# Kernel optimization log

Hardware: AMD Instinct MI355X
Metric: run time of the kernel (lower is better)

## Reference

```python
import jax, jax.numpy as jnp
from jax import lax
import numpy as np

HIDDEN = 512
INPUT = 64
ALPHA = 1.0 / 10.0  # dt / tau = 1.0 / 10.0


def setup_inputs() -> dict:
    key = jax.random.key(0)
    k1, k2, k3, k4, k5, k6 = jax.random.split(key, 6)
    inputs = jax.random.normal(k1, (64, INPUT), dtype=jnp.float32)
    # Linear params (torch convention: y = x @ W.T + b)
    W_in = jax.random.normal(k2, (HIDDEN, INPUT), dtype=jnp.float32) / np.sqrt(INPUT)
    b_in = jax.random.normal(k3, (HIDDEN,), dtype=jnp.float32) * 0.01
    W_rec = jax.random.normal(k4, (HIDDEN, HIDDEN), dtype=jnp.float32) / np.sqrt(HIDDEN)
    w_out = jax.random.normal(k5, (1, HIDDEN), dtype=jnp.float32) / np.sqrt(HIDDEN)
    b_out = jax.random.normal(k6, (1,), dtype=jnp.float32) * 0.01
    return {
        "inputs": inputs,
        "W_in": W_in,
        "b_in": b_in,
        "W_rec": W_rec,
        "w_out": w_out,
        "b_out": b_out,
        "warmup_steps": 100,
        "response_steps": 400,
        "num_trials": 8,
    }


def reference(inputs, W_in, b_in, W_rec, w_out, b_out, warmup_steps, response_steps, num_trials):
    batch_size = inputs.shape[0]
    # expand each batch row num_trials times (matches unsqueeze/expand/reshape)
    x = jnp.repeat(inputs, num_trials, axis=0)  # [B*T_trials, I]
    input_contribution = x @ W_in.T + b_in      # [E, H]
    h0 = jnp.zeros((batch_size * num_trials, HIDDEN), dtype=inputs.dtype)

    def step(h, _):
        rec = jax.nn.softplus(h) @ W_rec.T
        h = h * (1.0 - ALPHA) + ALPHA * (rec + input_contribution)
        return h, None

    h, _ = lax.scan(step, h0, None, length=warmup_steps)

    def step_collect(h, _):
        rec = jax.nn.softplus(h) @ W_rec.T
        h = h * (1.0 - ALPHA) + ALPHA * (rec + input_contribution)
        return h, h

    _, hs = lax.scan(step_collect, h, None, length=response_steps)  # [S, E, H]

    out = hs @ w_out[0] + b_out[0]            # [S, E]
    hazard = jax.nn.sigmoid(out)
    # [S, E] -> [E, S] -> [batch, trials, steps]
    hazard = hazard.T.reshape(batch_size, num_trials, response_steps)
    return hazard
```

## Files before the change

### kernel.cpp

```cpp
#include <hip/hip_runtime.h>
#include <math.h>

#define HIDDEN 512
#define INPUT  64
#define NB     64
#define NT     8
#define WARM   100
#define RESP   400
#define ALPHA  0.1f

#define NREGC  23
#define NLDSC  9

typedef _Float16 half8  __attribute__((ext_vector_type(8)));
typedef _Float16 half2v __attribute__((ext_vector_type(2)));

#if defined(__has_builtin)
#  if __has_builtin(__builtin_amdgcn_fdot2)
#    define HAS_FDOT2 1
#  endif
#endif

__device__ __forceinline__ void dot8(half8 w, half8 s, float& a0, float& a1) {
#ifdef HAS_FDOT2
  a0 = __builtin_amdgcn_fdot2(__builtin_shufflevector(w, w, 0, 1),
                              __builtin_shufflevector(s, s, 0, 1), a0, false);
  a1 = __builtin_amdgcn_fdot2(__builtin_shufflevector(w, w, 2, 3),
                              __builtin_shufflevector(s, s, 2, 3), a1, false);
  a0 = __builtin_amdgcn_fdot2(__builtin_shufflevector(w, w, 4, 5),
                              __builtin_shufflevector(s, s, 4, 5), a0, false);
  a1 = __builtin_amdgcn_fdot2(__builtin_shufflevector(w, w, 6, 7),
                              __builtin_shufflevector(s, s, 6, 7), a1, false);
#else
#pragma unroll
  for (int l = 0; l < 8; ++l)
    ((l & 1) ? a1 : a0) = fmaf((float)w[l], (float)s[l], (l & 1) ? a1 : a0);
#endif
}

__device__ __forceinline__ void dot8f(float w0, float w1, float w2, float w3,
                                      half8 s, float& a0, float& a1) {
#ifdef HAS_FDOT2
  a0 = __builtin_amdgcn_fdot2(__builtin_bit_cast(half2v, w0),
                              __builtin_shufflevector(s, s, 0, 1), a0, false);
  a1 = __builtin_amdgcn_fdot2(__builtin_bit_cast(half2v, w1),
                              __builtin_shufflevector(s, s, 2, 3), a1, false);
  a0 = __builtin_amdgcn_fdot2(__builtin_bit_cast(half2v, w2),
                              __builtin_shufflevector(s, s, 4, 5), a0, false);
  a1 = __builtin_amdgcn_fdot2(__builtin_bit_cast(half2v, w3),
                              __builtin_shufflevector(s, s, 6, 7), a1, false);
#else
  const float wf[4] = {w0, w1, w2, w3};
#pragma unroll
  for (int p = 0; p < 4; ++p) {
    half2v wp = __builtin_bit_cast(half2v, wf[p]);
    float& a = (p & 1) ? a1 : a0;
    a = fmaf((float)wp[0], (float)s[2 * p], a);
    a = fmaf((float)wp[1], (float)s[2 * p + 1], a);
  }
#endif
}

__global__ void convert_w_pack_kernel(const float* __restrict__ W,
                                      _Float16* __restrict__ Wpk) {
  const int t = blockIdx.x * blockDim.x + threadIdx.x;
  const int kblk = t & 63;
  const int j = t >> 6;
  const float* src = W + (size_t)j * HIDDEN + kblk * 8;
  _Float16* dst = Wpk + ((size_t)kblk * HIDDEN + j) * 8;
#pragma unroll
  for (int l = 0; l < 8; ++l) dst[l] = (_Float16)src[l];
}

__global__ void
__attribute__((amdgpu_flat_work_group_size(1024, 1024), amdgpu_waves_per_eu(4, 4)))
leaky_rnn_res_kernel(const float* __restrict__ inputs,
                     const float* __restrict__ W_in,
                     const float* __restrict__ b_in,
                     const _Float16* __restrict__ Wpk,
                     const float* __restrict__ w_out,
                     const float* __restrict__ b_out,
                     float* __restrict__ out ) {
  const int b = blockIdx.x;
  const int t = threadIdx.x;
  const int j = t & (HIDDEN - 1);
  const int kh = t >> 9;

  __shared__ __align__(16) half8 ldsW[NLDSC][1024];
  __shared__ __align__(16) _Float16 sp_h[HIDDEN];
  __shared__ float xin[INPUT];
  __shared__ float redk[HIDDEN];
  __shared__ float wsum[8];

  const half8* __restrict__ Wp8 =
      (const half8*)Wpk + (size_t)(kh * 32) * HIDDEN + j;
  const float4* __restrict__ Wp4 = (const float4*)Wp8;

  float wrf[NREGC * 4];
#pragma unroll
  for (int c = 0; c < NREGC; ++c) {
    float4 v = Wp4[(size_t)c * HIDDEN];
    wrf[4 * c + 0] = v.x;
    wrf[4 * c + 1] = v.y;
    wrf[4 * c + 2] = v.z;
    wrf[4 * c + 3] = v.w;
    asm volatile("" : "+v"(wrf[4 * c + 0]), "+v"(wrf[4 * c + 1]),
                      "+v"(wrf[4 * c + 2]), "+v"(wrf[4 * c + 3]));
  }
#pragma unroll
  for (int c = 0; c < NLDSC; ++c) ldsW[c][t] = Wp8[(size_t)(NREGC + c) * HIDDEN];

  if (t < INPUT) xin[t] = inputs[b * INPUT + t];
  __syncthreads();

  float ic = 0.f, wout = 0.f;
  const float bout = b_out[0];
  if (t < HIDDEN) {
    ic = b_in[j];
    const float* wi = W_in + (size_t)j * INPUT;
#pragma unroll
    for (int i = 0; i < INPUT; ++i) ic = fmaf(xin[i], wi[i], ic);
    wout = w_out[j];
    sp_h[j] = (_Float16)0.6931471805599453f;
  }
  float h = 0.f;
  __syncthreads();

  const half8* sp8 = ((const half8*)sp_h) + kh * 32;
  float* const ob = out + (size_t)b * (NT * RESP) + (t < NT ? t * RESP : 0);

  for (int step = 0; step < WARM + RESP; ++step) {
    float acc0 = 0.f, acc1 = 0.f;
#pragma unroll
    for (int c = 0; c < NLDSC; ++c) {
      half8 w = ldsW[c][t];
      half8 s = sp8[NREGC + c];
      dot8(w, s, acc0, acc1);
    }
#pragma unroll
    for (int c = 0; c < NREGC; ++c) {
      half8 s = sp8[c];
      dot8f(wrf[4 * c + 0], wrf[4 * c + 1], wrf[4 * c + 2], wrf[4 * c + 3],
            s, acc0, acc1);
    }
    const float acc = acc0 + acc1;

    if (t >= HIDDEN) redk[j] = acc;
    __syncthreads();

    if (t < HIDDEN) {
      const float rec = acc + redk[j];
      h = h * (1.f - ALPHA) + ALPHA * (rec + ic);
      const float sp = fmaxf(h, 0.f) + log1pf(expf(-fabsf(h)));
      sp_h[j] = (_Float16)sp;
      if (step >= WARM) {
        float v = h * wout;
#pragma unroll
        for (int off = 32; off > 0; off >>= 1) v += __shfl_down(v, off);
        if ((t & 63) == 0) wsum[t >> 6] = v;
      }
    }
    __syncthreads();

    if (step >= WARM && t < NT) {
      float o = bout;
#pragma unroll
      for (int w = 0; w < 8; ++w) o += wsum[w];
      const float hz = 1.f / (1.f + expf(-o));
      ob[step - WARM] = hz;
    }
  }
}

__global__ void __launch_bounds__(512, 1)
leaky_rnn_row_kernel(const float* __restrict__ inputs,
                     const float* __restrict__ W_in,
                     const float* __restrict__ b_in,
                     const float* __restrict__ W_rec,
                     const float* __restrict__ w_out,
                     const float* __restrict__ b_out,
                     float* __restrict__ out) {
  const int b = blockIdx.x;
  const int j = threadIdx.x;
  __shared__ float sp[HIDDEN];
  __shared__ float xin[INPUT];
  __shared__ float red[8];
  if (j < INPUT) xin[j] = inputs[b * INPUT + j];
  __syncthreads();
  float ic = b_in[j];
  const float* wi = W_in + j * INPUT;
#pragma unroll
  for (int i = 0; i < INPUT; ++i) ic = fmaf(xin[i], wi[i], ic);
  const float wout = w_out[j];
  const float bout = b_out[0];
  float h = 0.0f;
  sp[j] = 0.6931471805599453f;
  __syncthreads();
  const float4* __restrict__ Wr = (const float4*)(W_rec + (size_t)j * HIDDEN);
  for (int step = 0; step < WARM + RESP; ++step) {
    float rec = 0.0f;
#pragma unroll 8
    for (int k4 = 0; k4 < HIDDEN / 4; ++k4) {
      float4 w = Wr[k4];
      float4 s = *(const float4*)&sp[4 * k4];
      rec = fmaf(w.x, s.x, rec);
      rec = fmaf(w.y, s.y, rec);
      rec = fmaf(w.z, s.z, rec);
      rec = fmaf(w.w, s.w, rec);
    }
    h = h * (1.0f - ALPHA) + ALPHA * (rec + ic);
    if (step >= WARM) {
      float v = h * wout;
#pragma unroll
      for (int off = 32; off > 0; off >>= 1) v += __shfl_down(v, off);
      if ((j & 63) == 0) red[j >> 6] = v;
    }
    __syncthreads();
    sp[j] = fmaxf(h, 0.0f) + log1pf(expf(-fabsf(h)));
    if (step >= WARM && j == 0) {
      float o = bout;
#pragma unroll
      for (int w = 0; w < 8; ++w) o += red[w];
      const float hz = 1.0f / (1.0f + expf(-o));
      const int s = step - WARM;
      float* obp = out + (size_t)b * (NT * RESP) + s;
#pragma unroll
      for (int tr = 0; tr < NT; ++tr) obp[tr * RESP] = hz;
    }
    __syncthreads();
  }
}

extern "C" void kernel_launch(void* const* d_in, const int* in_sizes, int n_in,
                              void* d_out, int out_size, void* d_ws, size_t ws_size,
                              hipStream_t stream) {
  const float* inputs = (const float*)d_in[0];
  const float* W_in   = (const float*)d_in[1];
  const float* b_in   = (const float*)d_in[2];
  const float* W_rec  = (const float*)d_in[3];
  const float* w_out  = (const float*)d_in[4];
  const float* b_out  = (const float*)d_in[5];
  float* out = (float*)d_out;

  const int nW = HIDDEN * HIDDEN;
  if (ws_size >= (size_t)nW * sizeof(_Float16)) {
    _Float16* Wpk = (_Float16*)d_ws;
    convert_w_pack_kernel<<<dim3(HIDDEN * 64 / 256), dim3(256), 0, stream>>>(W_rec, Wpk);
    leaky_rnn_res_kernel<<<dim3(NB), dim3(2 * HIDDEN), 0, stream>>>(
        inputs, W_in, b_in, Wpk, w_out, b_out, out);
  } else {
    leaky_rnn_row_kernel<<<dim3(NB), dim3(HIDDEN), 0, stream>>>(
        inputs, W_in, b_in, W_rec, w_out, b_out, out);
  }
}
```

Measured before the change: 1.085 ms.

## Split each batch row across four workgroups with global-memory flag synchronization

Adds a quad kernel where each batch row is handled by four cooperating workgroups, each owning 128 hidden units with its fp16 slice of W_rec fully resident in LDS. Every step the workgroups exchange softplus values and partial output sums through global memory, using relaxed atomics and per-step flag spinning. This spreads the work over 256 workgroups instead of 64 and removes the register-held weight tile. The cost is a cross-workgroup round trip through global memory every step, and it relies on all 256 workgroups being resident at once to avoid deadlock; the spin loop has a guard that breaks out after a bounded count.

```diff
diff --git a/kernel.cpp b/kernel.cpp
--- a/kernel.cpp
+++ b/kernel.cpp
@@ -7,10 +7,8 @@
 #define NT     8
 #define WARM   100
 #define RESP   400
+#define STEPS  (WARM + RESP)
 #define ALPHA  0.1f
-
-#define NREGC  23
-#define NLDSC  9
 
 typedef _Float16 half8  __attribute__((ext_vector_type(8)));
 typedef _Float16 half2v __attribute__((ext_vector_type(2)));
@@ -36,6 +34,148 @@
   for (int l = 0; l < 8; ++l)
     ((l & 1) ? a1 : a0) = fmaf((float)w[l], (float)s[l], (l & 1) ? a1 : a0);
 #endif
+}
+
+#define OFF_W    0
+#define OFF_SPEX (512 * 1024)
+#define OFF_OSUM (OFF_SPEX + NB * HIDDEN * 4)
+#define OFF_FLAG (OFF_OSUM + 1024)
+#define WS_NEED  (OFF_FLAG + 1024)
+
+__global__ void stage_quad_kernel(const float* __restrict__ W,
+                                  _Float16* __restrict__ Wst) {
+  const int gid = blockIdx.x * blockDim.x + threadIdx.x;
+  const int q  = gid >> 13;
+  const int c  = (gid >> 10) & 7;
+  const int tm = gid & 1023;
+  const int jg = q * 128 + (tm >> 3);
+  const int kb = (tm & 7) * 64 + c * 8;
+  const float* src = W + (size_t)jg * HIDDEN + kb;
+  _Float16* dst = Wst + ((size_t)(q * 8 + c) * 1024 + tm) * 8;
+#pragma unroll
+  for (int l = 0; l < 8; ++l) dst[l] = (_Float16)src[l];
+}
+
+__global__ void __launch_bounds__(1024)
+leaky_rnn_quad_kernel(const float* __restrict__ inputs,
+                      const float* __restrict__ W_in,
+                      const float* __restrict__ b_in,
+                      const _Float16* __restrict__ Wst,
+                      const float* __restrict__ w_out,
+                      const float* __restrict__ b_out,
+                      unsigned* __restrict__ sp_ex,
+                      unsigned* __restrict__ osum_ex,
+                      unsigned* __restrict__ flags,
+                      float* __restrict__ out ) {
+  const int wg = blockIdx.x;
+  const int r = wg & 63;
+  const int q = wg >> 6;
+  const int t = threadIdx.x;
+  const int jl = t >> 3;
+  const int kq = t & 7;
+  const int jg = q * 128 + jl;
+
+  __shared__ __align__(16) _Float16 ldsW[8 * 1024 * 8];
+  __shared__ __align__(16) _Float16 spst[2][8 * 72];
+  __shared__ float xin[INPUT];
+  __shared__ float wsum[16];
+
+  half8* ldsW8 = (half8*)ldsW;
+  const half8* Ws = (const half8*)Wst + (size_t)q * 8 * 1024;
+#pragma unroll
+  for (int c = 0; c < 8; ++c) ldsW8[c * 1024 + t] = Ws[c * 1024 + t];
+
+  if (t < INPUT) xin[t] = inputs[r * INPUT + t];
+  if (t < 8 * 72) spst[0][t] = (_Float16)0.6931471805599453f;
+  __syncthreads();
+
+  float ic = b_in[jg];
+  const float* wi = W_in + (size_t)jg * INPUT;
+#pragma unroll
+  for (int i = 0; i < INPUT; ++i) ic = fmaf(xin[i], wi[i], ic);
+  const float wout = w_out[jg];
+  const float bout = b_out[0];
+  float h = 0.f;
+
+  unsigned* const spex_r = sp_ex + r * HIDDEN;
+  unsigned* const osum_r = osum_ex + r * 4;
+  unsigned* const flag_r = flags + r * 4;
+  float* const ob = out + (size_t)r * (NT * RESP);
+
+  for (int step = 0; step < STEPS; ++step) {
+    const int p = step & 1;
+    const _Float16* spg = &spst[p][kq * 72];
+
+    float a0 = 0.f, a1 = 0.f;
+#pragma unroll
+    for (int c = 0; c < 8; ++c) {
+      half8 w = ldsW8[c * 1024 + t];
+      half8 s = *(const half8*)(spg + c * 8);
+      dot8(w, s, a0, a1);
+    }
+    float d = a0 + a1;
+    d += __shfl_xor(d, 1);
+    d += __shfl_xor(d, 2);
+    d += __shfl_xor(d, 4);
+
+    h = h * (1.f - ALPHA) + ALPHA * (d + ic);
+    const float spf = fmaxf(h, 0.f) + log1pf(expf(-fabsf(h)));
+
+    if (kq == 0) {
+      spst[1 - p][(jg >> 6) * 72 + (jg & 63)] = (_Float16)spf;
+      __hip_atomic_store(&spex_r[jg], __builtin_bit_cast(unsigned, spf),
+                         __ATOMIC_RELAXED, __HIP_MEMORY_SCOPE_AGENT);
+    }
+    if (step >= WARM) {
+      float v = (kq == 0) ? h * wout : 0.f;
+#pragma unroll
+      for (int off = 32; off; off >>= 1) v += __shfl_down(v, off);
+      if ((t & 63) == 0) wsum[t >> 6] = v;
+    }
+    __syncthreads();
+
+    if (t == 0) {
+      if (step >= WARM) {
+        float os = 0.f;
+#pragma unroll
+        for (int w = 0; w < 16; ++w) os += wsum[w];
+        __hip_atomic_store(&osum_r[q], __builtin_bit_cast(unsigned, os),
+                           __ATOMIC_RELAXED, __HIP_MEMORY_SCOPE_AGENT);
+      }
+      asm volatile("s_waitcnt vmcnt(0)" ::: "memory");
+      __hip_atomic_store(&flag_r[q], (unsigned)(step + 1),
+                         __ATOMIC_RELAXED, __HIP_MEMORY_SCOPE_AGENT);
+    }
+    if (t < 3) {
+      const int pq = t + (t >= q ? 1 : 0);
+      long guard = 0;
+      while (__hip_atomic_load(&flag_r[pq], __ATOMIC_RELAXED,
+                               __HIP_MEMORY_SCOPE_AGENT) <= (unsigned)step) {
+        if (++guard > (1L << 27)) break;
+      }
+    }
+    __syncthreads();
+
+    if (t < 384) {
+      const int k = t + (t >= q * 128 ? 128 : 0);
+      unsigned u = __hip_atomic_load(&spex_r[k], __ATOMIC_RELAXED,
+                                     __HIP_MEMORY_SCOPE_AGENT);
+      spst[1 - p][(k >> 6) * 72 + (k & 63)] =
+          (_Float16)__builtin_bit_cast(float, u);
+    }
+    if (step >= WARM && q == 0 && t == 0) {
+      float o = bout;
+#pragma unroll
+      for (int qq = 0; qq < 4; ++qq)
+        o += __builtin_bit_cast(
+            float, __hip_atomic_load(&osum_r[qq], __ATOMIC_RELAXED,
+                                     __HIP_MEMORY_SCOPE_AGENT));
+      const float hz = 1.f / (1.f + expf(-o));
+#pragma unroll
+      for (int tr = 0; tr < NT; ++tr) ob[tr * RESP + (step - WARM)] = hz;
+    }
+    __syncthreads();
+  }
 }
 
 __device__ __forceinline__ void dot8f(float w0, float w1, float w2, float w3,
@@ -52,14 +192,17 @@
 #else
   const float wf[4] = {w0, w1, w2, w3};
 #pragma unroll
-  for (int p = 0; p < 4; ++p) {
-    half2v wp = __builtin_bit_cast(half2v, wf[p]);
-    float& a = (p & 1) ? a1 : a0;
-    a = fmaf((float)wp[0], (float)s[2 * p], a);
-    a = fmaf((float)wp[1], (float)s[2 * p + 1], a);
+  for (int pp = 0; pp < 4; ++pp) {
+    half2v wp = __builtin_bit_cast(half2v, wf[pp]);
+    float& a = (pp & 1) ? a1 : a0;
+    a = fmaf((float)wp[0], (float)s[2 * pp], a);
+    a = fmaf((float)wp[1], (float)s[2 * pp + 1], a);
   }
 #endif
 }
+
+#define NREGC 23
+#define NLDSC 9
 
 __global__ void convert_w_pack_kernel(const float* __restrict__ W,
                                       _Float16* __restrict__ Wpk) {
@@ -72,15 +215,14 @@
   for (int l = 0; l < 8; ++l) dst[l] = (_Float16)src[l];
 }
 
-__global__ void
-__attribute__((amdgpu_flat_work_group_size(1024, 1024), amdgpu_waves_per_eu(4, 4)))
+__global__ void __launch_bounds__(1024)
 leaky_rnn_res_kernel(const float* __restrict__ inputs,
                      const float* __restrict__ W_in,
                      const float* __restrict__ b_in,
                      const _Float16* __restrict__ Wpk,
                      const float* __restrict__ w_out,
                      const float* __restrict__ b_out,
-                     float* __restrict__ out ) {
+                     float* __restrict__ out) {
   const int b = blockIdx.x;
   const int t = threadIdx.x;
   const int j = t & (HIDDEN - 1);
@@ -100,10 +242,8 @@
 #pragma unroll
   for (int c = 0; c < NREGC; ++c) {
     float4 v = Wp4[(size_t)c * HIDDEN];
-    wrf[4 * c + 0] = v.x;
-    wrf[4 * c + 1] = v.y;
-    wrf[4 * c + 2] = v.z;
-    wrf[4 * c + 3] = v.w;
+    wrf[4 * c + 0] = v.x; wrf[4 * c + 1] = v.y;
+    wrf[4 * c + 2] = v.z; wrf[4 * c + 3] = v.w;
     asm volatile("" : "+v"(wrf[4 * c + 0]), "+v"(wrf[4 * c + 1]),
                       "+v"(wrf[4 * c + 2]), "+v"(wrf[4 * c + 3]));
   }
@@ -129,21 +269,15 @@
   const half8* sp8 = ((const half8*)sp_h) + kh * 32;
   float* const ob = out + (size_t)b * (NT * RESP) + (t < NT ? t * RESP : 0);
 
-  for (int step = 0; step < WARM + RESP; ++step) {
-    float acc0 = 0.f, acc1 = 0.f;
-#pragma unroll
-    for (int c = 0; c < NLDSC; ++c) {
-      half8 w = ldsW[c][t];
-      half8 s = sp8[NREGC + c];
-      dot8(w, s, acc0, acc1);
-    }
-#pragma unroll
-    for (int c = 0; c < NREGC; ++c) {
-      half8 s = sp8[c];
+  for (int step = 0; step < STEPS; ++step) {
+    float a0 = 0.f, a1 = 0.f;
+#pragma unroll
+    for (int c = 0; c < NLDSC; ++c) dot8(ldsW[c][t], sp8[NREGC + c], a0, a1);
+#pragma unroll
+    for (int c = 0; c < NREGC; ++c)
       dot8f(wrf[4 * c + 0], wrf[4 * c + 1], wrf[4 * c + 2], wrf[4 * c + 3],
-            s, acc0, acc1);
-    }
-    const float acc = acc0 + acc1;
+            sp8[c], a0, a1);
+    const float acc = a0 + a1;
 
     if (t >= HIDDEN) redk[j] = acc;
     __syncthreads();
@@ -151,8 +285,7 @@
     if (t < HIDDEN) {
       const float rec = acc + redk[j];
       h = h * (1.f - ALPHA) + ALPHA * (rec + ic);
-      const float sp = fmaxf(h, 0.f) + log1pf(expf(-fabsf(h)));
-      sp_h[j] = (_Float16)sp;
+      sp_h[j] = (_Float16)(fmaxf(h, 0.f) + log1pf(expf(-fabsf(h))));
       if (step >= WARM) {
         float v = h * wout;
 #pragma unroll
@@ -166,8 +299,7 @@
       float o = bout;
 #pragma unroll
       for (int w = 0; w < 8; ++w) o += wsum[w];
-      const float hz = 1.f / (1.f + expf(-o));
-      ob[step - WARM] = hz;
+      ob[step - WARM] = 1.f / (1.f + expf(-o));
     }
   }
 }
@@ -197,16 +329,14 @@
   sp[j] = 0.6931471805599453f;
   __syncthreads();
   const float4* __restrict__ Wr = (const float4*)(W_rec + (size_t)j * HIDDEN);
-  for (int step = 0; step < WARM + RESP; ++step) {
+  for (int step = 0; step < STEPS; ++step) {
     float rec = 0.0f;
 #pragma unroll 8
     for (int k4 = 0; k4 < HIDDEN / 4; ++k4) {
       float4 w = Wr[k4];
       float4 s = *(const float4*)&sp[4 * k4];
-      rec = fmaf(w.x, s.x, rec);
-      rec = fmaf(w.y, s.y, rec);
-      rec = fmaf(w.z, s.z, rec);
-      rec = fmaf(w.w, s.w, rec);
+      rec = fmaf(w.x, s.x, rec); rec = fmaf(w.y, s.y, rec);
+      rec = fmaf(w.z, s.z, rec); rec = fmaf(w.w, s.w, rec);
     }
     h = h * (1.0f - ALPHA) + ALPHA * (rec + ic);
     if (step >= WARM) {
@@ -222,8 +352,7 @@
 #pragma unroll
       for (int w = 0; w < 8; ++w) o += red[w];
       const float hz = 1.0f / (1.0f + expf(-o));
-      const int s = step - WARM;
-      float* obp = out + (size_t)b * (NT * RESP) + s;
+      float* obp = out + (size_t)b * (NT * RESP) + (step - WARM);
 #pragma unroll
       for (int tr = 0; tr < NT; ++tr) obp[tr * RESP] = hz;
     }
@@ -242,8 +371,17 @@
   const float* b_out  = (const float*)d_in[5];
   float* out = (float*)d_out;
 
-  const int nW = HIDDEN * HIDDEN;
-  if (ws_size >= (size_t)nW * sizeof(_Float16)) {
+  if (ws_size >= (size_t)WS_NEED) {
+    char* ws = (char*)d_ws;
+    _Float16* Wst  = (_Float16*)(ws + OFF_W);
+    unsigned* spex = (unsigned*)(ws + OFF_SPEX);
+    unsigned* osum = (unsigned*)(ws + OFF_OSUM);
+    unsigned* flg  = (unsigned*)(ws + OFF_FLAG);
+    hipMemsetAsync(flg, 0, NB * 4 * sizeof(unsigned), stream);
+    stage_quad_kernel<<<dim3(128), dim3(256), 0, stream>>>(W_rec, Wst);
+    leaky_rnn_quad_kernel<<<dim3(256), dim3(1024), 0, stream>>>(
+        inputs, W_in, b_in, Wst, w_out, b_out, spex, osum, flg, out);
+  } else if (ws_size >= (size_t)HIDDEN * HIDDEN * sizeof(_Float16)) {
     _Float16* Wpk = (_Float16*)d_ws;
     convert_w_pack_kernel<<<dim3(HIDDEN * 64 / 256), dim3(256), 0, stream>>>(W_rec, Wpk);
     leaky_rnn_res_kernel<<<dim3(NB), dim3(2 * HIDDEN), 0, stream>>>(
```

After: 1.762 ms. +62.5%, slower.

## Split recurrent weights across AGPRs, global streaming, and LDS

Applied to the files above, without the earlier changes.

Weight residency changes. Before, 23 half8 chunks per thread sat in VGPRs and 9 in LDS. Now 16 chunks sit in AGPRs, read back with v_accvgpr_read each step, and 7 chunks are re-streamed from global/L2 every timestep, while LDS still holds 9. The aim is to free VGPR pressure and the waves_per_eu constraint. The cost is extra accvgpr reads, and per-step global loads that sit on the serial recurrence critical path.

```diff
diff --git a/kernel.cpp b/kernel.cpp
--- a/kernel.cpp
+++ b/kernel.cpp
@@ -7,9 +7,11 @@
 #define NT     8
 #define WARM   100
 #define RESP   400
+#define STEPS  (WARM + RESP)
 #define ALPHA  0.1f
 
-#define NREGC  23
+#define NAGPC  16
+#define NSTRC  7
 #define NLDSC  9
 
 typedef _Float16 half8  __attribute__((ext_vector_type(8)));
@@ -61,6 +63,15 @@
 #endif
 }
 
+__device__ __forceinline__ void ag_write(float& a, float v) {
+  asm volatile("v_accvgpr_write_b32 %0, %1" : "=a"(a) : "v"(v));
+}
+__device__ __forceinline__ float ag_read(const float& a) {
+  float v;
+  asm volatile("v_accvgpr_read_b32 %0, %1" : "=v"(v) : "a"(a));
+  return v;
+}
+
 __global__ void convert_w_pack_kernel(const float* __restrict__ W,
                                       _Float16* __restrict__ Wpk) {
   const int t = blockIdx.x * blockDim.x + threadIdx.x;
@@ -72,15 +83,14 @@
   for (int l = 0; l < 8; ++l) dst[l] = (_Float16)src[l];
 }
 
-__global__ void
-__attribute__((amdgpu_flat_work_group_size(1024, 1024), amdgpu_waves_per_eu(4, 4)))
-leaky_rnn_res_kernel(const float* __restrict__ inputs,
-                     const float* __restrict__ W_in,
-                     const float* __restrict__ b_in,
-                     const _Float16* __restrict__ Wpk,
-                     const float* __restrict__ w_out,
-                     const float* __restrict__ b_out,
-                     float* __restrict__ out ) {
+__global__ void __launch_bounds__(1024)
+leaky_rnn_ag_kernel(const float* __restrict__ inputs,
+                    const float* __restrict__ W_in,
+                    const float* __restrict__ b_in,
+                    const _Float16* __restrict__ Wpk,
+                    const float* __restrict__ w_out,
+                    const float* __restrict__ b_out,
+                    float* __restrict__ out ) {
   const int b = blockIdx.x;
   const int t = threadIdx.x;
   const int j = t & (HIDDEN - 1);
@@ -96,19 +106,18 @@
       (const half8*)Wpk + (size_t)(kh * 32) * HIDDEN + j;
   const float4* __restrict__ Wp4 = (const float4*)Wp8;
 
-  float wrf[NREGC * 4];
-#pragma unroll
-  for (int c = 0; c < NREGC; ++c) {
+  float ag[NAGPC * 4];
+#pragma unroll
+  for (int c = 0; c < NAGPC; ++c) {
     float4 v = Wp4[(size_t)c * HIDDEN];
-    wrf[4 * c + 0] = v.x;
-    wrf[4 * c + 1] = v.y;
-    wrf[4 * c + 2] = v.z;
-    wrf[4 * c + 3] = v.w;
-    asm volatile("" : "+v"(wrf[4 * c + 0]), "+v"(wrf[4 * c + 1]),
-                      "+v"(wrf[4 * c + 2]), "+v"(wrf[4 * c + 3]));
-  }
-#pragma unroll
-  for (int c = 0; c < NLDSC; ++c) ldsW[c][t] = Wp8[(size_t)(NREGC + c) * HIDDEN];
+    ag_write(ag[4 * c + 0], v.x);
+    ag_write(ag[4 * c + 1], v.y);
+    ag_write(ag[4 * c + 2], v.z);
+    ag_write(ag[4 * c + 3], v.w);
+  }
+#pragma unroll
+  for (int c = 0; c < NLDSC; ++c)
+    ldsW[c][t] = Wp8[(size_t)(NAGPC + NSTRC + c) * HIDDEN];
 
   if (t < INPUT) xin[t] = inputs[b * INPUT + t];
   __syncthreads();
@@ -129,21 +138,35 @@
   const half8* sp8 = ((const half8*)sp_h) + kh * 32;
   float* const ob = out + (size_t)b * (NT * RESP) + (t < NT ? t * RESP : 0);
 
-  for (int step = 0; step < WARM + RESP; ++step) {
-    float acc0 = 0.f, acc1 = 0.f;
-#pragma unroll
-    for (int c = 0; c < NLDSC; ++c) {
-      half8 w = ldsW[c][t];
-      half8 s = sp8[NREGC + c];
-      dot8(w, s, acc0, acc1);
-    }
-#pragma unroll
-    for (int c = 0; c < NREGC; ++c) {
-      half8 s = sp8[c];
-      dot8f(wrf[4 * c + 0], wrf[4 * c + 1], wrf[4 * c + 2], wrf[4 * c + 3],
-            s, acc0, acc1);
-    }
-    const float acc = acc0 + acc1;
+  for (int step = 0; step < STEPS; ++step) {
+    float4 st0 = Wp4[(size_t)(NAGPC + 0) * HIDDEN];
+    float4 st1 = Wp4[(size_t)(NAGPC + 1) * HIDDEN];
+    float4 st2 = Wp4[(size_t)(NAGPC + 2) * HIDDEN];
+    float4 st3 = Wp4[(size_t)(NAGPC + 3) * HIDDEN];
+    float4 st4 = Wp4[(size_t)(NAGPC + 4) * HIDDEN];
+    float4 st5 = Wp4[(size_t)(NAGPC + 5) * HIDDEN];
+    float4 st6 = Wp4[(size_t)(NAGPC + 6) * HIDDEN];
+
+    float a0 = 0.f, a1 = 0.f;
+#pragma unroll
+    for (int c = 0; c < NLDSC; ++c)
+      dot8(ldsW[c][t], sp8[NAGPC + NSTRC + c], a0, a1);
+#pragma unroll
+    for (int c = 0; c < NAGPC; ++c) {
+      float w0 = ag_read(ag[4 * c + 0]);
+      float w1 = ag_read(ag[4 * c + 1]);
+      float w2 = ag_read(ag[4 * c + 2]);
+      float w3 = ag_read(ag[4 * c + 3]);
+      dot8f(w0, w1, w2, w3, sp8[c], a0, a1);
+    }
+    dot8f(st0.x, st0.y, st0.z, st0.w, sp8[NAGPC + 0], a0, a1);
+    dot8f(st1.x, st1.y, st1.z, st1.w, sp8[NAGPC + 1], a0, a1);
+    dot8f(st2.x, st2.y, st2.z, st2.w, sp8[NAGPC + 2], a0, a1);
+    dot8f(st3.x, st3.y, st3.z, st3.w, sp8[NAGPC + 3], a0, a1);
+    dot8f(st4.x, st4.y, st4.z, st4.w, sp8[NAGPC + 4], a0, a1);
+    dot8f(st5.x, st5.y, st5.z, st5.w, sp8[NAGPC + 5], a0, a1);
+    dot8f(st6.x, st6.y, st6.z, st6.w, sp8[NAGPC + 6], a0, a1);
+    const float acc = a0 + a1;
 
     if (t >= HIDDEN) redk[j] = acc;
     __syncthreads();
@@ -197,16 +220,14 @@
   sp[j] = 0.6931471805599453f;
   __syncthreads();
   const float4* __restrict__ Wr = (const float4*)(W_rec + (size_t)j * HIDDEN);
-  for (int step = 0; step < WARM + RESP; ++step) {
+  for (int step = 0; step < STEPS; ++step) {
     float rec = 0.0f;
 #pragma unroll 8
     for (int k4 = 0; k4 < HIDDEN / 4; ++k4) {
       float4 w = Wr[k4];
       float4 s = *(const float4*)&sp[4 * k4];
-      rec = fmaf(w.x, s.x, rec);
-      rec = fmaf(w.y, s.y, rec);
-      rec = fmaf(w.z, s.z, rec);
-      rec = fmaf(w.w, s.w, rec);
+      rec = fmaf(w.x, s.x, rec); rec = fmaf(w.y, s.y, rec);
+      rec = fmaf(w.z, s.z, rec); rec = fmaf(w.w, s.w, rec);
     }
     h = h * (1.0f - ALPHA) + ALPHA * (rec + ic);
     if (step >= WARM) {
@@ -222,8 +243,7 @@
 #pragma unroll
       for (int w = 0; w < 8; ++w) o += red[w];
       const float hz = 1.0f / (1.0f + expf(-o));
-      const int s = step - WARM;
-      float* obp = out + (size_t)b * (NT * RESP) + s;
+      float* obp = out + (size_t)b * (NT * RESP) + (step - WARM);
 #pragma unroll
       for (int tr = 0; tr < NT; ++tr) obp[tr * RESP] = hz;
     }
@@ -246,7 +266,7 @@
   if (ws_size >= (size_t)nW * sizeof(_Float16)) {
     _Float16* Wpk = (_Float16*)d_ws;
     convert_w_pack_kernel<<<dim3(HIDDEN * 64 / 256), dim3(256), 0, stream>>>(W_rec, Wpk);
-    leaky_rnn_res_kernel<<<dim3(NB), dim3(2 * HIDDEN), 0, stream>>>(
+    leaky_rnn_ag_kernel<<<dim3(NB), dim3(2 * HIDDEN), 0, stream>>>(
         inputs, W_in, b_in, Wpk, w_out, b_out, out);
   } else {
     leaky_rnn_row_kernel<<<dim3(NB), dim3(HIDDEN), 0, stream>>>(
```

Result: slower. 1.295 ms (+19.4%).
